# Optimization experiments

Measured on AMD Instinct MI355X. Metric: run time of the kernel, lower is better.

The kernel has to match this reference:

```python
import jax, jax.numpy as jnp
import numpy as np
from jax import lax

B, T, L, HID = 128, 8, 8, 64  # batch, horizon(=num_layers), lstm layers, hidden

def setup_inputs() -> dict:
    key = jax.random.key(0)
    ks = jax.random.split(key, 40)
    def rn(i, shape, s=0.02):
        return jax.random.normal(ks[i], shape, dtype=jnp.float32) * s
    inp = {
        'image_data': jax.random.normal(ks[0], (B, 3, 192, 256), jnp.float32),
        'action_input_data': jax.random.normal(ks[1], (B, T, 2), jnp.float32),
        'ground_truth_data': jax.random.normal(ks[2], (B, T, 6), jnp.float32),
        'conv1_w': rn(3, (32, 3, 5, 5)), 'conv1_b': rn(4, (32,)),
        'conv2_w': rn(5, (64, 32, 3, 3)), 'conv2_b': rn(6, (64,)),
        'conv3_w': rn(7, (64, 64, 3, 3)), 'conv3_b': rn(8, (64,)),
        'fc1_w': rn(9, (256, 42240)), 'fc1_b': rn(10, (256,)),
        'fc2_w': rn(11, (128, 256)), 'fc2_b': rn(12, (128,)),
        'lowd1_w': rn(13, (128, 128)), 'lowd1_b': rn(14, (128,)),
        'lowd2_w': rn(15, (128, 128)), 'lowd2_b': rn(16, (128,)),
        'act1_w': rn(17, (16, 2)), 'act1_b': rn(18, (16,)),
        'act2_w': rn(19, (16, 16)), 'act2_b': rn(20, (16,)),
        'lstm_Wih0': rn(21, (4 * HID, 16)),
        'lstm_Wih': rn(22, (L - 1, 4 * HID, HID)),
        'lstm_Whh': rn(23, (L, 4 * HID, HID)),
        'lstm_bih': rn(24, (L, 4 * HID)),
        'lstm_bhh': rn(25, (L, 4 * HID)),
        'out1_w': rn(26, (32, 64)), 'out1_b': rn(27, (32,)),
        'out2_w': rn(28, (4, 32)), 'out2_b': rn(29, (4,)),
        'BATCH_SIZE': B, 'horizon': T,
    }
    return inp

def _lin(x, w, b):
    return x @ w.T + b

def _conv(x, w, b):
    y = lax.conv_general_dilated(x, w, (2, 2), 'VALID',
                                 dimension_numbers=('NCHW', 'OIHW', 'NCHW'))
    return y + b[None, :, None, None]

def _lstm(x, h0, c0, Wih0, Wih, Whh, bih, bhh):
    # x: (B,T,16); h0/c0: (L,B,HID). PyTorch gate order: i,f,g,o.
    inp = x
    for l in range(L):
        Wih_l = Wih0 if l == 0 else Wih[l - 1]
        bih_l, bhh_l, Whh_l = bih[l], bhh[l], Whh[l]
        def step(carry, xt):
            h, c = carry
            g = xt @ Wih_l.T + bih_l + h @ Whh_l.T + bhh_l
            i_, f_, g_, o_ = jnp.split(g, 4, axis=-1)
            c = jax.nn.sigmoid(f_) * c + jax.nn.sigmoid(i_) * jnp.tanh(g_)
            h = jax.nn.sigmoid(o_) * jnp.tanh(c)
            return (h, c), h
        _, ys = lax.scan(step, (h0[l], c0[l]), jnp.swapaxes(inp, 0, 1))
        inp = jnp.swapaxes(ys, 0, 1)  # (B,T,HID)
    return inp

def reference(image_data, action_input_data, ground_truth_data,
              conv1_w, conv1_b, conv2_w, conv2_b, conv3_w, conv3_b,
              fc1_w, fc1_b, fc2_w, fc2_b,
              lowd1_w, lowd1_b, lowd2_w, lowd2_b,
              act1_w, act1_b, act2_w, act2_b,
              lstm_Wih0, lstm_Wih, lstm_Whh, lstm_bih, lstm_bhh,
              out1_w, out1_b, out2_w, out2_b,
              BATCH_SIZE, horizon):
    # CNN image pipeline
    x = jax.nn.relu(_conv(image_data, conv1_w, conv1_b))
    x = jax.nn.relu(_conv(x, conv2_w, conv2_b))
    x = _conv(x, conv3_w, conv3_b)
    x = x.reshape(x.shape[0], -1)  # (B, 42240)
    x = jax.nn.relu(_lin(x, fc1_w, fc1_b))
    cnn_out1 = _lin(x, fc2_w, fc2_b)  # (B,128)
    cnn_out2 = _lin(jax.nn.relu(_lin(cnn_out1, lowd1_w, lowd1_b)), lowd2_w, lowd2_b)
    # action pipeline
    a = _lin(jax.nn.relu(_lin(action_input_data, act1_w, act1_b)), act2_w, act2_b)
    # split: first 64 -> c0, second 64 -> h0; broadcast over layers
    c_tmp, h_tmp = cnn_out2[:, :HID], cnn_out2[:, HID:]
    h0 = jnp.broadcast_to(h_tmp[None], (L, h_tmp.shape[0], HID))
    c0 = jnp.broadcast_to(c_tmp[None], (L, c_tmp.shape[0], HID))
    lstm_out = _lstm(a, h0, c0, lstm_Wih0, lstm_Wih, lstm_Whh, lstm_bih, lstm_bhh)
    mo = _lin(jax.nn.relu(_lin(lstm_out, out1_w, out1_b)), out2_w, out2_b)  # (B,T,4)
    # batched yaw rotation (vectorizes the original per-sample loop)
    yaw = ground_truth_data[:, 0, 5]
    cy, sy = jnp.cos(yaw), jnp.sin(yaw)
    z, o = jnp.zeros_like(cy), jnp.ones_like(cy)
    rot = jnp.stack([cy, -sy, z, sy, cy, z, z, z, o], axis=-1).reshape(-1, 3, 3)
    pos = jnp.einsum('bti,bij->btj', mo[:, :, :3], rot) + ground_truth_data[:, 0, 1:4][:, None, :]
    return jnp.concatenate([pos, mo[:, :, 3:4]], axis=-1)
```

## Files before the change

### kernel.cpp

```cpp
#include <hip/hip_runtime.h>
#include <cstdint>

#define DEV __device__ __forceinline__

typedef __attribute__((ext_vector_type(8))) short bf16x8;
typedef __attribute__((ext_vector_type(4))) float f32x4;
typedef __attribute__((ext_vector_type(2))) __fp16 h2t;
typedef __attribute__((ext_vector_type(4))) unsigned int u32x4;
typedef unsigned long long u64;

DEV unsigned short f2bf(float f) {
    unsigned u = __float_as_uint(f);
    unsigned r = u + 0x7fffu + ((u >> 16) & 1u);
    return (unsigned short)(r >> 16);
}
DEV uint32_t pkbf2(float a, float b) {
    return (uint32_t)f2bf(a) | ((uint32_t)f2bf(b) << 16);
}
DEV uint32_t pkh2(float a, float b) {
    h2t p = __builtin_amdgcn_cvt_pkrtz(a, b);
    union { h2t h; uint32_t u; } c;
    c.h = p;
    return c.u;
}
DEV float dot2(uint32_t w, uint32_t x, float acc) {
    union { uint32_t u; h2t h; } a, b;
    a.u = w; b.u = x;
    return __builtin_amdgcn_fdot2(a.h, b.h, acc, false);
}
DEV float sigm(float x) { return __builtin_amdgcn_rcpf(1.f + __expf(-x)); }
DEV float tanh_(float x) { return fmaf(2.f, sigm(2.f * x), -1.f); }
DEV uint32_t packpair(float h) {
    float hs = __int_as_float(__builtin_amdgcn_ds_swizzle(__float_as_int(h), 0x041F));
    return pkh2(h, hs);
}
DEV uint32_t comp4v(u32x4 v, int e) {
    return (e == 0) ? v[0] : (e == 1) ? v[1] : (e == 2) ? v[2] : v[3];
}
DEV u64 pack4bf(float a, float b, float c, float d) {
    unsigned lo = (unsigned)f2bf(a) | ((unsigned)f2bf(b) << 16);
    unsigned hi = (unsigned)f2bf(c) | ((unsigned)f2bf(d) << 16);
    return (u64)lo | ((u64)hi << 32);
}

__global__ __launch_bounds__(256) void k_wprep(const float* __restrict__ w1,
                                               const float* __restrict__ w2,
                                               const float* __restrict__ w3,
                                               unsigned short* __restrict__ w1t,
                                               unsigned short* __restrict__ w2t,
                                               unsigned short* __restrict__ w3t) {
    int i = blockIdx.x * 256 + threadIdx.x;
    if (i < 32 * 128) {
        int oc = i >> 7, k = i & 127;
        int cc = k >> 3, u = (k >> 2) & 1, c = k & 3;
        int r = cc / 3, kx = 2 * (cc - 3 * r) + u;
        w1t[i] = (cc < 15 && kx < 5 && c < 3) ? f2bf(w1[oc * 75 + c * 25 + r * 5 + kx])
                                              : (unsigned short)0;
    } else if (i < 32 * 128 + 64 * 288) {
        int j = i - 32 * 128;
        int oc = j / 288, k = j - oc * 288;
        int pos = k >> 5, c = k & 31;
        int ocr = ((c >> 2) & 1) * 16 + (c >> 3) * 4 + (c & 3);
        w2t[j] = f2bf(w2[oc * 288 + ocr * 9 + pos]);
    } else if (i < 32 * 128 + 64 * 288 + 64 * 576) {
        int j = i - 32 * 128 - 64 * 288;
        int oc = j / 576, k = j - oc * 576;
        int pos = k >> 6, c = k & 63;
        w3t[j] = f2bf(w3[oc * 576 + c * 9 + pos]);
    }
}

__global__ __launch_bounds__(256) void k_wprep_lstm(const float* __restrict__ Wih0,
                                                    const float* __restrict__ Wih,
                                                    const float* __restrict__ Whh,
                                                    uint32_t* __restrict__ wpk) {
    int idx = blockIdx.x * 256 + threadIdx.x;
    int lane = idx & 63;
    int j = (idx >> 6) & 63;
    int l = idx >> 12;
    int g = j >> 4, q = j & 15;
    int r = g * 64 + lane;
    uint32_t ov[4];
#pragma unroll
    for (int e = 0; e < 4; ++e) {
        int p = q * 4 + e;
        float w0, w1;
        if (p < 32) {
            int k0 = 2 * p;
            if (l == 0) {
                w0 = (k0 < 16) ? Wih0[r * 16 + k0] : 0.f;
                w1 = (k0 + 1 < 16) ? Wih0[r * 16 + k0 + 1] : 0.f;
            } else {
                const float* base = Wih + ((size_t)(l - 1) * 256 + r) * 64;
                w0 = base[k0];
                w1 = base[k0 + 1];
            }
        } else {
            int k0 = 2 * (p - 32);
            const float* base = Whh + ((size_t)l * 256 + r) * 64;
            w0 = base[k0];
            w1 = base[k0 + 1];
        }
        ov[e] = pkh2(w0, w1);
    }
    uint4 v;
    v.x = ov[0]; v.y = ov[1]; v.z = ov[2]; v.w = ov[3];
    ((uint4*)wpk)[idx] = v;
}

__global__ __launch_bounds__(256, 1) void k_conv12(const float* __restrict__ img,
                                                   const unsigned short* __restrict__ w1t,
                                                   const float* __restrict__ b1,
                                                   const unsigned short* __restrict__ w2t,
                                                   const float* __restrict__ b2,
                                                   unsigned short* __restrict__ out) {
    int b = blockIdx.x, xh = blockIdx.y, yh = blockIdx.z;
    int tid = threadIdx.x;
    int w = tid >> 6, lane = tid & 63;
    int quad = lane >> 4, nl = lane & 15;
    int nh = w >> 1, rw = w & 1;
    __shared__ __align__(16) char ldsI[8 * 2080];
    __shared__ __align__(16) char ldsC[4 * 4536];
    const float* ib = img + (size_t)b * 3 * 192 * 256;
    int y0 = yh * 23;
    int imx = 124 * xh + tid;
    bool stg = tid < 132;

    bf16x8 wa1[4], wb1[4];
#pragma unroll
    for (int ks = 0; ks < 4; ++ks) {
        wa1[ks] = *(const bf16x8*)(w1t + nl * 128 + ks * 32 + quad * 8);
        wb1[ks] = *(const bf16x8*)(w1t + (16 + nl) * 128 + ks * 32 + quad * 8);
    }
    bf16x8 wa2[9], wb2[9];
#pragma unroll
    for (int ks = 0; ks < 9; ++ks) {
        wa2[ks] = *(const bf16x8*)(w2t + ((rw * 2 + 0) * 16 + nl) * 288 + ks * 32 + quad * 8);
        wb2[ks] = *(const bf16x8*)(w2t + ((rw * 2 + 1) * 16 + nl) * 288 + ks * 32 + quad * 8);
    }
    float4 c1b0 = *(const float4*)(b1 + quad * 4);
    float4 c1b1 = *(const float4*)(b1 + 16 + quad * 4);
    float4 c2b0 = *(const float4*)(b2 + (rw * 2 + 0) * 16 + quad * 4);
    float4 c2b1 = *(const float4*)(b2 + (rw * 2 + 1) * 16 + quad * 4);

    auto ldimg = [&](int row, float& f0, float& f1, float& f2) {
        if (row > 191) row = 191;
        const float* ip = ib + row * 256 + imx;
        f0 = ip[0];
        f1 = ip[192 * 256];
        f2 = ip[2 * 192 * 256];
    };
    auto stimg = [&](int row, float f0, float f1, float f2) {
        uint32_t lo = (uint32_t)f2bf(f0) | ((uint32_t)f2bf(f1) << 16);
        *(u64*)(ldsI + (row & 7) * 2080 + imx * 8) = (u64)lo | ((u64)f2bf(f2) << 32);
    };
    auto conv1row = [&](int R1) {
        f32x4 a00, a01;
        a00[0] = c1b0.x; a00[1] = c1b0.y; a00[2] = c1b0.z; a00[3] = c1b0.w;
        a01[0] = c1b1.x; a01[1] = c1b1.y; a01[2] = c1b1.z; a01[3] = c1b1.w;
        f32x4 a10 = a00, a11 = a01;
#pragma unroll
        for (int ks = 0; ks < 4; ++ks) {
            int cc = ks * 4 + quad;
            int r = cc / 3, kxp = cc - 3 * r;
            int rb = ((2 * R1 + r) & 7) * 2080 + 992 * xh + 512 * nh + kxp * 16 + nl * 16;
            bf16x8 v0 = *(const bf16x8*)(ldsI + rb);
            bf16x8 v1 = *(const bf16x8*)(ldsI + rb + 256);
            a00 = __builtin_amdgcn_mfma_f32_16x16x32_bf16(wa1[ks], v0, a00, 0, 0, 0);
            a01 = __builtin_amdgcn_mfma_f32_16x16x32_bf16(wb1[ks], v0, a01, 0, 0, 0);
            a10 = __builtin_amdgcn_mfma_f32_16x16x32_bf16(wa1[ks], v1, a10, 0, 0, 0);
            a11 = __builtin_amdgcn_mfma_f32_16x16x32_bf16(wb1[ks], v1, a11, 0, 0, 0);
        }
        int cs = (R1 & 3) * 4536;
        int xl0 = nh * 32 + nl;
        {
            u64 lo = pack4bf(fmaxf(a00[0], 0.f), fmaxf(a00[1], 0.f),
                             fmaxf(a00[2], 0.f), fmaxf(a00[3], 0.f));
            u64 hi = pack4bf(fmaxf(a01[0], 0.f), fmaxf(a01[1], 0.f),
                             fmaxf(a01[2], 0.f), fmaxf(a01[3], 0.f));
            uint4 st;
            st.x = (uint32_t)lo; st.y = (uint32_t)(lo >> 32);
            st.z = (uint32_t)hi; st.w = (uint32_t)(hi >> 32);
            *(uint4*)(ldsC + cs + xl0 * 72 + quad * 16) = st;
        }
        int xl1 = xl0 + 16;
        if (xl1 < 63) {
            u64 lo = pack4bf(fmaxf(a10[0], 0.f), fmaxf(a10[1], 0.f),
                             fmaxf(a10[2], 0.f), fmaxf(a10[3], 0.f));
            u64 hi = pack4bf(fmaxf(a11[0], 0.f), fmaxf(a11[1], 0.f),
                             fmaxf(a11[2], 0.f), fmaxf(a11[3], 0.f));
            uint4 st;
            st.x = (uint32_t)lo; st.y = (uint32_t)(lo >> 32);
            st.z = (uint32_t)hi; st.w = (uint32_t)(hi >> 32);
            *(uint4*)(ldsC + cs + xl1 * 72 + quad * 16) = st;
        }
    };

    {
        float p0[8], p1[8], p2[8];
        if (stg) {
#pragma unroll
            for (int r = 0; r < 8; ++r) ldimg(4 * y0 + r, p0[r], p1[r], p2[r]);
        }
        __builtin_amdgcn_sched_barrier(0);
        if (stg) {
#pragma unroll
            for (int r = 0; r < 8; ++r) stimg(4 * y0 + r, p0[r], p1[r], p2[r]);
        }
    }
    __syncthreads();
    conv1row(2 * y0 + rw);
    float g0[4], g1[4], g2[4];
    if (stg) {
#pragma unroll
        for (int r = 0; r < 4; ++r) ldimg(4 * y0 + 8 + r, g0[r], g1[r], g2[r]);
    }
    __syncthreads();
    if (stg) {
#pragma unroll
        for (int r = 0; r < 4; ++r) stimg(4 * y0 + 8 + r, g0[r], g1[r], g2[r]);
    }
    __syncthreads();

    for (int t = 0; t < 23; ++t) {
        int y = y0 + t;
        conv1row(2 * y + 2 + rw);
        if (stg) {
#pragma unroll
            for (int r = 0; r < 4; ++r) ldimg(4 * y + 12 + r, g0[r], g1[r], g2[r]);
        }
        __syncthreads();
        {
            f32x4 acc0, acc1;
            acc0[0] = c2b0.x; acc0[1] = c2b0.y; acc0[2] = c2b0.z; acc0[3] = c2b0.w;
            acc1[0] = c2b1.x; acc1[1] = c2b1.y; acc1[2] = c2b1.z; acc1[3] = c2b1.w;
            int xl = nh * 16 + nl;
#pragma unroll
            for (int ks = 0; ks < 9; ++ks) {
                int r = ks / 3, kx = ks - r * 3;
                const char* base = ldsC + ((2 * y + r) & 3) * 4536 + (2 * xl + kx) * 72 + quad * 16;
                union { u64 d[2]; bf16x8 v; } bb;
                bb.d[0] = *(const u64*)(base);
                bb.d[1] = *(const u64*)(base + 8);
                acc0 = __builtin_amdgcn_mfma_f32_16x16x32_bf16(wa2[ks], bb.v, acc0, 0, 0, 0);
                acc1 = __builtin_amdgcn_mfma_f32_16x16x32_bf16(wb2[ks], bb.v, acc1, 0, 0, 0);
            }
            if (xl < 31) {
                int xg = xh * 31 + xl;
                u64 q0 = pack4bf(fmaxf(acc0[0], 0.f), fmaxf(acc0[1], 0.f),
                                 fmaxf(acc0[2], 0.f), fmaxf(acc0[3], 0.f));
                u64 q1 = pack4bf(fmaxf(acc1[0], 0.f), fmaxf(acc1[1], 0.f),
                                 fmaxf(acc1[2], 0.f), fmaxf(acc1[3], 0.f));
                *(u64*)(out + (((size_t)b * 46 + y) * 62 + xg) * 64 + (rw * 2 + 0) * 16 + quad * 4) = q0;
                *(u64*)(out + (((size_t)b * 46 + y) * 62 + xg) * 64 + (rw * 2 + 1) * 16 + quad * 4) = q1;
            }
        }
        if (stg) {
#pragma unroll
            for (int r = 0; r < 4; ++r) stimg(4 * y + 12 + r, g0[r], g1[r], g2[r]);
        }
        __syncthreads();
    }
}

__global__ __launch_bounds__(256, 1) void k_conv3m(const unsigned short* __restrict__ in,
                                                   const unsigned short* __restrict__ w3t,
                                                   const float* __restrict__ bias,
                                                   unsigned short* __restrict__ out) {
    int b = blockIdx.x, xh = blockIdx.y, yh = blockIdx.z;
    int tid = threadIdx.x;
    int wave = tid >> 6, lane = tid & 63;
    int quad = lane >> 4, nl = lane & 15;
    __shared__ __align__(16) char lds[4 * 4488];
    const u64* in64 = (const u64*)in;

    bf16x8 wf[18];
#pragma unroll
    for (int ks = 0; ks < 18; ++ks)
        wf[ks] = *(const bf16x8*)(w3t + (wave * 16 + nl) * 576 + ks * 32 + quad * 8);
    float4 bv = *(const float4*)(bias + wave * 16 + quad * 4);

    int y0 = yh * 11;
    int rr = tid >> 7, li = tid & 127;

    {
        int y2 = 2 * y0 + rr;
        const u64* s = in64 + ((size_t)(b * 46 + y2) * 62 + 30 * xh) * 16;
        int slot = y2 & 3;
        u64 g0[4];
#pragma unroll
        for (int j = 0; j < 4; ++j) { int idx = li + j * 128; g0[j] = (idx < 496) ? s[idx] : 0ull; }
#pragma unroll
        for (int j = 0; j < 4; ++j) {
            int idx = li + j * 128;
            if (idx < 496) *(u64*)(lds + slot * 4488 + (idx >> 4) * 136 + (idx & 15) * 8) = g0[j];
        }
        int y2b = 2 * y0 + 2;
        const u64* s2 = in64 + ((size_t)(b * 46 + y2b) * 62 + 30 * xh) * 16;
        int slot2 = y2b & 3;
        u64 g1[2];
#pragma unroll
        for (int j = 0; j < 2; ++j) { int idx = tid + j * 256; g1[j] = (idx < 496) ? s2[idx] : 0ull; }
#pragma unroll
        for (int j = 0; j < 2; ++j) {
            int idx = tid + j * 256;
            if (idx < 496) *(u64*)(lds + slot2 * 4488 + (idx >> 4) * 136 + (idx & 15) * 8) = g1[j];
        }
    }
    u64 g[4];
    {
        int y2 = 2 * y0 + 3 + rr;
        const u64* s = in64 + ((size_t)(b * 46 + y2) * 62 + 30 * xh) * 16;
#pragma unroll
        for (int j = 0; j < 4; ++j) { int idx = li + j * 128; g[j] = (idx < 496) ? s[idx] : 0ull; }
    }
    __syncthreads();

    for (int yy = 0; yy < 11; ++yy) {
        int y = y0 + yy;
        f32x4 acc;
        acc[0] = bv.x; acc[1] = bv.y; acc[2] = bv.z; acc[3] = bv.w;
        int sb0 = ((2 * y) & 3) * 4488;
        int sb1 = ((2 * y + 1) & 3) * 4488;
        int sb2 = ((2 * y + 2) & 3) * 4488;
#pragma unroll
        for (int ks = 0; ks < 18; ++ks) {
            const int pos = ks >> 1, half = ks & 1;
            const int r = pos / 3, kx = pos - r * 3;
            int sb = (r == 0) ? sb0 : (r == 1) ? sb1 : sb2;
            union { u64 d[2]; bf16x8 v; } bb;
            const char* base = lds + sb + (2 * nl + kx) * 136 + half * 64 + quad * 16;
            bb.d[0] = *(const u64*)(base);
            bb.d[1] = *(const u64*)(base + 8);
            acc = __builtin_amdgcn_mfma_f32_16x16x32_bf16(wf[ks], bb.v, acc, 0, 0, 0);
        }
        if (nl < 15) {
            int xg = xh * 15 + nl;
#pragma unroll
            for (int r2 = 0; r2 < 4; ++r2)
                out[(size_t)b * 42240 + (wave * 16 + quad * 4 + r2) * 660 + y * 30 + xg] = f2bf(acc[r2]);
        }
        __syncthreads();
        {
            int row = 2 * y + 3 + rr;
            int slot = row & 3;
#pragma unroll
            for (int j = 0; j < 4; ++j) {
                int idx = li + j * 128;
                if (idx < 496) *(u64*)(lds + slot * 4488 + (idx >> 4) * 136 + (idx & 15) * 8) = g[j];
            }
        }
        if (yy < 10) {
            int y2 = 2 * y + 5 + rr;
            if (y2 > 45) y2 = 45;
            const u64* s = in64 + ((size_t)(b * 46 + y2) * 62 + 30 * xh) * 16;
#pragma unroll
            for (int j = 0; j < 4; ++j) { int idx = li + j * 128; g[j] = (idx < 496) ? s[idx] : 0ull; }
        }
        __syncthreads();
    }
}

__global__ __launch_bounds__(256) void k_fc1_mfma(const unsigned short* __restrict__ A,
                                                  const float* __restrict__ W,
                                                  float* __restrict__ part) {
    int kc = blockIdx.x;
    int nb = blockIdx.y;
    int tid = threadIdx.x;
    int wave = tid >> 6, lane = tid & 63;
    int m16 = lane & 15, quad = lane >> 4;
    __shared__ __align__(16) char lw[2][64 * 80];
    __shared__ __align__(16) char la[2][128 * 80];
    int k0 = kc * 704;
    int wrow = tid >> 2, wseg = tid & 3;
    const float* wsrc = W + (size_t)(nb * 64 + wrow) * 42240 + k0 + wseg * 8;
    int arow = tid >> 1, aseg = tid & 1;
    const uint4* asrc = (const uint4*)(A + (size_t)arow * 42240 + k0) + aseg * 2;
    float4 wr0 = ((const float4*)wsrc)[0];
    float4 wr1 = ((const float4*)wsrc)[1];
    uint4 ar0 = asrc[0];
    uint4 ar1 = asrc[1];
    f32x4 acc[8] = {};
    for (int ks = 0; ks < 22; ++ks) {
        int buf = ks & 1;
        uint4 wp;
        wp.x = pkbf2(wr0.x, wr0.y); wp.y = pkbf2(wr0.z, wr0.w);
        wp.z = pkbf2(wr1.x, wr1.y); wp.w = pkbf2(wr1.z, wr1.w);
        *(uint4*)(lw[buf] + wrow * 80 + wseg * 16) = wp;
        *(uint4*)(la[buf] + arow * 80 + aseg * 32) = ar0;
        *(uint4*)(la[buf] + arow * 80 + aseg * 32 + 16) = ar1;
        if (ks < 21) {
            wsrc += 32;
            asrc += 4;
            wr0 = ((const float4*)wsrc)[0];
            wr1 = ((const float4*)wsrc)[1];
            ar0 = asrc[0];
            ar1 = asrc[1];
        }
        __syncthreads();
        bf16x8 wf = *(const bf16x8*)(lw[buf] + (wave * 16 + m16) * 80 + quad * 16);
        const char* lab = la[buf] + m16 * 80 + quad * 16;
#pragma unroll
        for (int tm = 0; tm < 8; ++tm) {
            bf16x8 af = *(const bf16x8*)(lab + tm * 16 * 80);
            acc[tm] = __builtin_amdgcn_mfma_f32_16x16x32_bf16(af, wf, acc[tm], 0, 0, 0);
        }
    }
    int n = nb * 64 + wave * 16 + m16;
    float* pb = part + ((size_t)kc * 128) * 256 + n;
#pragma unroll
    for (int tm = 0; tm < 8; ++tm) {
        int row = tm * 16 + quad * 4;
#pragma unroll
        for (int r = 0; r < 4; ++r) pb[(size_t)(row + r) * 256] = acc[tm][r];
    }
}

__global__ __launch_bounds__(256) void k_head(const float* __restrict__ part,
                                              const float* __restrict__ f1b,
                                              const float* __restrict__ w2, const float* __restrict__ b2,
                                              const float* __restrict__ lw1, const float* __restrict__ lb1,
                                              const float* __restrict__ lw2, const float* __restrict__ lb2,
                                              float* __restrict__ cnn2) {
    int b = blockIdx.x, t = threadIdx.x;
    __shared__ float xa[256];
    __shared__ float xb[128];
    __shared__ float xc[128];
    __shared__ float pp[256];
    float s = f1b[t];
#pragma unroll
    for (int kc = 0; kc < 60; ++kc) s += part[((size_t)kc * 128 + b) * 256 + t];
    xa[t] = fmaxf(s, 0.f);
    __syncthreads();
    int n = t & 127, half = t >> 7;
    float acc = half ? 0.f : b2[n];
    {
        const float* w2r = w2 + n * 256 + half * 128;
        const float* xar = xa + half * 128;
#pragma unroll
        for (int k = 0; k < 128; ++k) acc = fmaf(xar[k], w2r[k], acc);
    }
    pp[t] = acc;
    __syncthreads();
    if (t < 128) xb[t] = pp[t] + pp[t + 128];
    __syncthreads();
    acc = half ? 0.f : lb1[n];
    {
        const float* l1r = lw1 + n * 128 + half * 64;
        const float* xbr = xb + half * 64;
#pragma unroll
        for (int k = 0; k < 64; ++k) acc = fmaf(xbr[k], l1r[k], acc);
    }
    pp[t] = acc;
    __syncthreads();
    if (t < 128) xc[t] = fmaxf(pp[t] + pp[t + 128], 0.f);
    __syncthreads();
    acc = half ? 0.f : lb2[n];
    {
        const float* l2r = lw2 + n * 128 + half * 64;
        const float* xcr = xc + half * 64;
#pragma unroll
        for (int k = 0; k < 64; ++k) acc = fmaf(xcr[k], l2r[k], acc);
    }
    pp[t] = acc;
    __syncthreads();
    if (t < 128) cnn2[b * 128 + t] = pp[t] + pp[t + 128];
}

__global__ __launch_bounds__(256) void k_act(const float* __restrict__ ain,
                                             const float* __restrict__ w1, const float* __restrict__ b1,
                                             const float* __restrict__ w2, const float* __restrict__ b2,
                                             float* __restrict__ abuf) {
    int idx = blockIdx.x * 256 + threadIdx.x;
    float x0 = ain[idx * 2], x1 = ain[idx * 2 + 1];
    float h1[16];
#pragma unroll
    for (int i = 0; i < 16; ++i)
        h1[i] = fmaxf(fmaf(x0, w1[i * 2], fmaf(x1, w1[i * 2 + 1], b1[i])), 0.f);
#pragma unroll
    for (int i = 0; i < 16; ++i) {
        float a = b2[i];
#pragma unroll
        for (int j = 0; j < 16; ++j) a = fmaf(h1[j], w2[i * 16 + j], a);
        abuf[idx * 16 + i] = a;
    }
}

__global__ __launch_bounds__(512, 2) void k_lstm(const float* __restrict__ abuf,
                                                 const float* __restrict__ cnn2,
                                                 const uint32_t* __restrict__ wpk,
                                                 const float* __restrict__ bih,
                                                 const float* __restrict__ bhh,
                                                 float* __restrict__ lout) {
    int b = blockIdx.x;
    int tid = threadIdx.x;
    int w = tid >> 6, lane = tid & 63;
    int sl = w >> 1, pt = w & 1;
    __shared__ uint32_t hbuf[2][3][32];
    __shared__ uint32_t h3pk[8][32];
    __shared__ float4 pex[8][64];

    uint32_t xq[8];
#pragma unroll
    for (int t = 0; t < 8; ++t) {
        float x0 = 0.f, x1 = 0.f;
        if (lane < 8) {
            const float* ap = abuf + (b * 8 + t) * 16 + 2 * lane;
            x0 = ap[0];
            x1 = ap[1];
        }
        xq[t] = pkh2(x0, x1);
    }
    float h0 = cnn2[b * 128 + 64 + lane];
    float c0 = cnn2[b * 128 + lane];
    const u32x4* wbase = (const u32x4*)wpk;

#pragma unroll
    for (int P = 0; P < 2; ++P) {
        const int L = P * 4 + sl;
        u32x4 wreg[4][8];
#pragma unroll
        for (int g = 0; g < 4; ++g)
#pragma unroll
            for (int q = 0; q < 8; ++q)
                wreg[g][q] = wbase[(size_t)L * 4096 + (g * 16 + pt * 8 + q) * 64 + lane];
        float bias0 = 0.f, bias1 = 0.f, bias2 = 0.f, bias3 = 0.f;
        if (pt == 0) {
            bias0 = bih[L * 256 + lane] + bhh[L * 256 + lane];
            bias1 = bih[L * 256 + 64 + lane] + bhh[L * 256 + 64 + lane];
            bias2 = bih[L * 256 + 128 + lane] + bhh[L * 256 + 128 + lane];
            bias3 = bih[L * 256 + 192 + lane] + bhh[L * 256 + 192 + lane];
        }
        float h = h0, c = c0;
        uint32_t hpk = packpair(h0);

        for (int s = 0; s < 11; ++s) {
            bool act = (s >= sl && s < sl + 8);
            float a0 = bias0, a1 = bias1, a2 = bias2, a3 = bias3;
            if (act) {
                if (pt == 0) {
                    uint32_t xcur;
                    if (sl == 0)
                        xcur = (P == 0) ? xq[0] : h3pk[s][lane & 31];
                    else
                        xcur = hbuf[(s & 1) ^ 1][sl - 1][lane & 31];
#pragma unroll
                    for (int m = 0; m < 32; ++m) {
                        uint32_t bx = (uint32_t)__builtin_amdgcn_readlane((int)xcur, m);
                        int q = m >> 2, e = m & 3;
                        a0 = dot2(comp4v(wreg[0][q], e), bx, a0);
                        a1 = dot2(comp4v(wreg[1][q], e), bx, a1);
                        a2 = dot2(comp4v(wreg[2][q], e), bx, a2);
                        a3 = dot2(comp4v(wreg[3][q], e), bx, a3);
                    }
                } else {
#pragma unroll
                    for (int m = 0; m < 32; ++m) {
                        uint32_t bh2 = (uint32_t)__builtin_amdgcn_readlane((int)hpk, 2 * m);
                        int q = m >> 2, e = m & 3;
                        a0 = dot2(comp4v(wreg[0][q], e), bh2, a0);
                        a1 = dot2(comp4v(wreg[1][q], e), bh2, a1);
                        a2 = dot2(comp4v(wreg[2][q], e), bh2, a2);
                        a3 = dot2(comp4v(wreg[3][q], e), bh2, a3);
                    }
                }
                float4 pv;
                pv.x = a0; pv.y = a1; pv.z = a2; pv.w = a3;
                pex[w][lane] = pv;
            }
            __syncthreads();
            if (act) {
                float4 po = pex[w ^ 1][lane];
                float g0 = a0 + po.x, g1 = a1 + po.y, g2 = a2 + po.z, g3 = a3 + po.w;
                float gi = sigm(g0), gf = sigm(g1), gv = tanh_(g2), go = sigm(g3);
                c = gf * c + gi * gv;
                h = go * tanh_(c);
                hpk = packpair(h);
                if (pt == 0) {
                    if (sl < 3) {
                        if (!(lane & 1)) hbuf[s & 1][sl][lane >> 1] = hpk;
                    } else if (P == 0) {
                        if (!(lane & 1)) h3pk[s - 3][lane >> 1] = hpk;
                    } else {
                        lout[((size_t)b * 8 + (s - 3)) * 64 + lane] = h;
                    }
                }
            }
            if (P == 0 && w == 0) {
#pragma unroll
                for (int k = 0; k < 7; ++k) xq[k] = xq[k + 1];
            }
            __syncthreads();
        }
    }
}

__global__ __launch_bounds__(256) void k_out(const float* __restrict__ lout,
                                             const float* __restrict__ w1, const float* __restrict__ b1,
                                             const float* __restrict__ w2, const float* __restrict__ b2,
                                             const float* __restrict__ gt, float* __restrict__ out) {
    int idx = blockIdx.x * 256 + threadIdx.x;
    int b = idx >> 3;
    float x[64];
#pragma unroll
    for (int j = 0; j < 64; ++j) x[j] = lout[idx * 64 + j];
    float h[32];
#pragma unroll 8
    for (int i = 0; i < 32; ++i) {
        float a = b1[i];
#pragma unroll
        for (int j = 0; j < 64; ++j) a = fmaf(x[j], w1[i * 64 + j], a);
        h[i] = fmaxf(a, 0.f);
    }
    float mo[4];
#pragma unroll
    for (int i = 0; i < 4; ++i) {
        float a = b2[i];
#pragma unroll
        for (int j = 0; j < 32; ++j) a = fmaf(h[j], w2[i * 32 + j], a);
        mo[i] = a;
    }
    float yaw = gt[b * 48 + 5];
    float cy = cosf(yaw), sy = sinf(yaw);
    out[idx * 4 + 0] = fmaf(mo[0], cy, fmaf(mo[1], sy, gt[b * 48 + 1]));
    out[idx * 4 + 1] = fmaf(mo[0], -sy, fmaf(mo[1], cy, gt[b * 48 + 2]));
    out[idx * 4 + 2] = mo[2] + gt[b * 48 + 3];
    out[idx * 4 + 3] = mo[3];
}

extern "C" void kernel_launch(void* const* d_in, const int* in_sizes, int n_in,
                              void* d_out, int out_size, void* d_ws, size_t ws_size,
                              hipStream_t stream) {
    const float* img = (const float*)d_in[0];
    const float* ain = (const float*)d_in[1];
    const float* gt = (const float*)d_in[2];
    const float* c1w = (const float*)d_in[3];
    const float* c1b = (const float*)d_in[4];
    const float* c2w = (const float*)d_in[5];
    const float* c2b = (const float*)d_in[6];
    const float* c3w = (const float*)d_in[7];
    const float* c3b = (const float*)d_in[8];
    const float* f1w = (const float*)d_in[9];
    const float* f1b = (const float*)d_in[10];
    const float* f2w = (const float*)d_in[11];
    const float* f2b = (const float*)d_in[12];
    const float* l1w = (const float*)d_in[13];
    const float* l1b = (const float*)d_in[14];
    const float* l2w = (const float*)d_in[15];
    const float* l2b = (const float*)d_in[16];
    const float* a1w = (const float*)d_in[17];
    const float* a1b = (const float*)d_in[18];
    const float* a2w = (const float*)d_in[19];
    const float* a2b = (const float*)d_in[20];
    const float* wih0 = (const float*)d_in[21];
    const float* wih = (const float*)d_in[22];
    const float* whh = (const float*)d_in[23];
    const float* bihp = (const float*)d_in[24];
    const float* bhhp = (const float*)d_in[25];
    const float* o1w = (const float*)d_in[26];
    const float* o1b = (const float*)d_in[27];
    const float* o2w = (const float*)d_in[28];
    const float* o2b = (const float*)d_in[29];
    float* out = (float*)d_out;

    char* ws = (char*)d_ws;
    unsigned short* c2o = (unsigned short*)(ws + 97026048);
    unsigned short* c3o = (unsigned short*)(ws + 143753216);
    float* f1p = (float*)(ws + 154566656);
    float* cnn2 = (float*)(ws + 163348480);
    float* abuf = (float*)(ws + 163414016);
    float* lo = (float*)(ws + 163479552);
    unsigned short* w1t = (unsigned short*)(ws + 163741696);
    unsigned short* w2t = (unsigned short*)(ws + 163749888);
    unsigned short* w3t = (unsigned short*)(ws + 163786752);
    uint32_t* wpk = (uint32_t*)(ws + 163860480);

    k_wprep<<<232, 256, 0, stream>>>(c1w, c2w, c3w, w1t, w2t, w3t);
    k_wprep_lstm<<<128, 256, 0, stream>>>(wih0, wih, whh, wpk);
    k_conv12<<<dim3(128, 2, 2), 256, 0, stream>>>(img, w1t, c1b, w2t, c2b, c2o);
    k_conv3m<<<dim3(128, 2, 2), 256, 0, stream>>>(c2o, w3t, c3b, c3o);
    k_fc1_mfma<<<dim3(60, 4), 256, 0, stream>>>(c3o, f1w, f1p);
    k_head<<<128, 256, 0, stream>>>(f1p, f1b, f2w, f2b, l1w, l1b, l2w, l2b, cnn2);
    k_act<<<4, 256, 0, stream>>>(ain, a1w, a1b, a2w, a2b, abuf);
    k_lstm<<<128, 512, 0, stream>>>(abuf, cnn2, wpk, bihp, bhhp, lo);
    k_out<<<4, 256, 0, stream>>>(lo, o1w, o1b, o2w, o2b, gt, out);
}
```

Before: 331.8 us.

## Split conv1+conv2 into four row slices with deeper ring buffers and one barrier per step

The fused conv1/conv2 kernel now splits output rows into four slices instead of two, doubling the grid to 1024 blocks, and allows two blocks per CU. The image and conv1 staging buffers become 12- and 6-slot rings. One conv1 row is computed ahead so each loop step needs only one barrier instead of two. The aim is more parallelism and fewer synchronisations per row, at the cost of more LDS per block, more recomputed halo rows at slice edges, and more complex slot indexing.

```diff
diff --git a/kernel.cpp b/kernel.cpp
--- a/kernel.cpp
+++ b/kernel.cpp
@@ -108,21 +108,22 @@
     ((uint4*)wpk)[idx] = v;
 }
 
-__global__ __launch_bounds__(256, 1) void k_conv12(const float* __restrict__ img,
+__global__ __launch_bounds__(256, 2) void k_conv12(const float* __restrict__ img,
                                                    const unsigned short* __restrict__ w1t,
                                                    const float* __restrict__ b1,
                                                    const unsigned short* __restrict__ w2t,
                                                    const float* __restrict__ b2,
                                                    unsigned short* __restrict__ out) {
-    int b = blockIdx.x, xh = blockIdx.y, yh = blockIdx.z;
+    int b = blockIdx.x, xh = blockIdx.y, ys = blockIdx.z;
     int tid = threadIdx.x;
     int w = tid >> 6, lane = tid & 63;
     int quad = lane >> 4, nl = lane & 15;
     int nh = w >> 1, rw = w & 1;
-    __shared__ __align__(16) char ldsI[8 * 2080];
-    __shared__ __align__(16) char ldsC[4 * 4536];
+    __shared__ __align__(16) char ldsI[12 * 2080];
+    __shared__ __align__(16) char ldsC[6 * 4536];
     const float* ib = img + (size_t)b * 3 * 192 * 256;
-    int y0 = yh * 23;
+    int y0 = ys * 12;
+    int NT = (ys == 3) ? 10 : 12;
     int imx = 124 * xh + tid;
     bool stg = tid < 132;
 
@@ -150,11 +151,11 @@
         f1 = ip[192 * 256];
         f2 = ip[2 * 192 * 256];
     };
-    auto stimg = [&](int row, float f0, float f1, float f2) {
+    auto stimgS = [&](int slot, float f0, float f1, float f2) {
         uint32_t lo = (uint32_t)f2bf(f0) | ((uint32_t)f2bf(f1) << 16);
-        *(u64*)(ldsI + (row & 7) * 2080 + imx * 8) = (u64)lo | ((u64)f2bf(f2) << 32);
+        *(u64*)(ldsI + slot * 2080 + imx * 8) = (u64)lo | ((u64)f2bf(f2) << 32);
     };
-    auto conv1row = [&](int R1) {
+    auto conv1row = [&](int s0, int cslot) {
         f32x4 a00, a01;
         a00[0] = c1b0.x; a00[1] = c1b0.y; a00[2] = c1b0.z; a00[3] = c1b0.w;
         a01[0] = c1b1.x; a01[1] = c1b1.y; a01[2] = c1b1.z; a01[3] = c1b1.w;
@@ -163,7 +164,8 @@
         for (int ks = 0; ks < 4; ++ks) {
             int cc = ks * 4 + quad;
             int r = cc / 3, kxp = cc - 3 * r;
-            int rb = ((2 * R1 + r) & 7) * 2080 + 992 * xh + 512 * nh + kxp * 16 + nl * 16;
+            int sl = s0 + r; if (sl >= 12) sl -= 12;
+            int rb = sl * 2080 + 992 * xh + 512 * nh + kxp * 16 + nl * 16;
             bf16x8 v0 = *(const bf16x8*)(ldsI + rb);
             bf16x8 v1 = *(const bf16x8*)(ldsI + rb + 256);
             a00 = __builtin_amdgcn_mfma_f32_16x16x32_bf16(wa1[ks], v0, a00, 0, 0, 0);
@@ -171,7 +173,7 @@
             a10 = __builtin_amdgcn_mfma_f32_16x16x32_bf16(wa1[ks], v1, a10, 0, 0, 0);
             a11 = __builtin_amdgcn_mfma_f32_16x16x32_bf16(wb1[ks], v1, a11, 0, 0, 0);
         }
-        int cs = (R1 & 3) * 4536;
+        int cs = cslot * 4536;
         int xl0 = nh * 32 + nl;
         {
             u64 lo = pack4bf(fmaxf(a00[0], 0.f), fmaxf(a00[1], 0.f),
@@ -197,39 +199,46 @@
     };
 
     {
-        float p0[8], p1[8], p2[8];
+        float p0[12], p1[12], p2[12];
         if (stg) {
 #pragma unroll
-            for (int r = 0; r < 8; ++r) ldimg(4 * y0 + r, p0[r], p1[r], p2[r]);
+            for (int r = 0; r < 12; ++r) ldimg(4 * y0 + r, p0[r], p1[r], p2[r]);
         }
         __builtin_amdgcn_sched_barrier(0);
         if (stg) {
 #pragma unroll
-            for (int r = 0; r < 8; ++r) stimg(4 * y0 + r, p0[r], p1[r], p2[r]);
-        }
-    }
-    __syncthreads();
-    conv1row(2 * y0 + rw);
+            for (int r = 0; r < 12; ++r) stimgS(r, p0[r], p1[r], p2[r]);
+        }
+    }
+    __syncthreads();
+    conv1row(2 * rw, rw);
     float g0[4], g1[4], g2[4];
     if (stg) {
 #pragma unroll
-        for (int r = 0; r < 4; ++r) ldimg(4 * y0 + 8 + r, g0[r], g1[r], g2[r]);
-    }
-    __syncthreads();
+        for (int j = 0; j < 4; ++j) ldimg(4 * y0 + 12 + j, g0[j], g1[j], g2[j]);
+    }
+    __syncthreads();
+    conv1row(4 + 2 * rw, 2 + rw);
     if (stg) {
 #pragma unroll
-        for (int r = 0; r < 4; ++r) stimg(4 * y0 + 8 + r, g0[r], g1[r], g2[r]);
-    }
-    __syncthreads();
-
-    for (int t = 0; t < 23; ++t) {
+        for (int j = 0; j < 4; ++j) stimgS(j, g0[j], g1[j], g2[j]);
+    }
+    __syncthreads();
+
+    int t3 = 0;
+    for (int t = 0; t < NT; ++t) {
         int y = y0 + t;
-        conv1row(2 * y + 2 + rw);
+        int t3h = t3 >> 1;
         if (stg) {
 #pragma unroll
-            for (int r = 0; r < 4; ++r) ldimg(4 * y + 12 + r, g0[r], g1[r], g2[r]);
-        }
-        __syncthreads();
+            for (int j = 0; j < 4; ++j) ldimg(4 * y + 16 + j, g0[j], g1[j], g2[j]);
+        }
+        int R1 = 2 * y + 4 + rw;
+        if (R1 <= 93) {
+            int s0 = t3 + 8 + 2 * rw; if (s0 >= 12) s0 -= 12;
+            int cs = t3h + 4 + rw; if (cs >= 6) cs -= 6;
+            conv1row(s0, cs);
+        }
         {
             f32x4 acc0, acc1;
             acc0[0] = c2b0.x; acc0[1] = c2b0.y; acc0[2] = c2b0.z; acc0[3] = c2b0.w;
@@ -238,7 +247,8 @@
 #pragma unroll
             for (int ks = 0; ks < 9; ++ks) {
                 int r = ks / 3, kx = ks - r * 3;
-                const char* base = ldsC + ((2 * y + r) & 3) * 4536 + (2 * xl + kx) * 72 + quad * 16;
+                int cs = t3h + r; if (cs >= 6) cs -= 6;
+                const char* base = ldsC + cs * 4536 + (2 * xl + kx) * 72 + quad * 16;
                 union { u64 d[2]; bf16x8 v; } bb;
                 bb.d[0] = *(const u64*)(base);
                 bb.d[1] = *(const u64*)(base + 8);
@@ -257,9 +267,13 @@
         }
         if (stg) {
 #pragma unroll
-            for (int r = 0; r < 4; ++r) stimg(4 * y + 12 + r, g0[r], g1[r], g2[r]);
+            for (int j = 0; j < 4; ++j) {
+                int sl = t3 + 4 + j; if (sl >= 12) sl -= 12;
+                stimgS(sl, g0[j], g1[j], g2[j]);
+            }
         }
         __syncthreads();
+        t3 += 4; if (t3 == 12) t3 = 0;
     }
 }
 
@@ -677,7 +691,7 @@
 
     k_wprep<<<232, 256, 0, stream>>>(c1w, c2w, c3w, w1t, w2t, w3t);
     k_wprep_lstm<<<128, 256, 0, stream>>>(wih0, wih, whh, wpk);
-    k_conv12<<<dim3(128, 2, 2), 256, 0, stream>>>(img, w1t, c1b, w2t, c2b, c2o);
+    k_conv12<<<dim3(128, 2, 4), 256, 0, stream>>>(img, w1t, c1b, w2t, c2b, c2o);
     k_conv3m<<<dim3(128, 2, 2), 256, 0, stream>>>(c2o, w3t, c3b, c3o);
     k_fc1_mfma<<<dim3(60, 4), 256, 0, stream>>>(c3o, f1w, f1p);
     k_head<<<128, 256, 0, stream>>>(f1p, f1b, f2w, f2b, l1w, l1b, l2w, l2b, cnn2);
```

Result: no change. 327.0 us (-1.4%).

## Deepen conv1/conv2 LDS ring buffers and prefetch image rows two stages ahead

Applied to the files above, without the earlier changes.

The fused conv1+conv2 kernel now uses 16-row image and 8-row conv1 LDS rings. Image rows are loaded two iterations ahead with ping-pong registers, which removes one of the two __syncthreads per output row. The software bf16 rounding is replaced by the hardware v_cvt_pk_bf16_f32 instruction, and launch bounds ask for 2 blocks per CU. LDS per block roughly doubles (about 69KB), which may limit co-residency, and the 2-block hint may add register pressure or spilling.

```diff
diff --git a/kernel.cpp b/kernel.cpp
--- a/kernel.cpp
+++ b/kernel.cpp
@@ -16,6 +16,11 @@
 }
 DEV uint32_t pkbf2(float a, float b) {
     return (uint32_t)f2bf(a) | ((uint32_t)f2bf(b) << 16);
+}
+DEV uint32_t cvtpk(float lo, float hi) {
+    uint32_t r;
+    asm("v_cvt_pk_bf16_f32 %0, %1, %2" : "=v"(r) : "v"(lo), "v"(hi));
+    return r;
 }
 DEV uint32_t pkh2(float a, float b) {
     h2t p = __builtin_amdgcn_cvt_pkrtz(a, b);
@@ -108,21 +113,21 @@
     ((uint4*)wpk)[idx] = v;
 }
 
-__global__ __launch_bounds__(256, 1) void k_conv12(const float* __restrict__ img,
+__global__ __launch_bounds__(256, 2) void k_conv12(const float* __restrict__ img,
                                                    const unsigned short* __restrict__ w1t,
                                                    const float* __restrict__ b1,
                                                    const unsigned short* __restrict__ w2t,
                                                    const float* __restrict__ b2,
                                                    unsigned short* __restrict__ out) {
-    int b = blockIdx.x, xh = blockIdx.y, yh = blockIdx.z;
+    int b = blockIdx.x, xh = blockIdx.y, ys = blockIdx.z;
     int tid = threadIdx.x;
     int w = tid >> 6, lane = tid & 63;
     int quad = lane >> 4, nl = lane & 15;
     int nh = w >> 1, rw = w & 1;
-    __shared__ __align__(16) char ldsI[8 * 2080];
-    __shared__ __align__(16) char ldsC[4 * 4536];
+    __shared__ __align__(16) char ldsI[16 * 2080];
+    __shared__ __align__(16) char ldsC[8 * 4536];
     const float* ib = img + (size_t)b * 3 * 192 * 256;
-    int y0 = yh * 23;
+    int y0 = ys * 23;
     int imx = 124 * xh + tid;
     bool stg = tid < 132;
 
@@ -150,20 +155,21 @@
         f1 = ip[192 * 256];
         f2 = ip[2 * 192 * 256];
     };
-    auto stimg = [&](int row, float f0, float f1, float f2) {
-        uint32_t lo = (uint32_t)f2bf(f0) | ((uint32_t)f2bf(f1) << 16);
-        *(u64*)(ldsI + (row & 7) * 2080 + imx * 8) = (u64)lo | ((u64)f2bf(f2) << 32);
+    auto stimgS = [&](int row, float f0, float f1, float f2) {
+        uint32_t lo = cvtpk(f0, f1);
+        *(u64*)(ldsI + (row & 15) * 2080 + imx * 8) = (u64)lo | ((u64)cvtpk(f2, 0.f) << 32);
     };
     auto conv1row = [&](int R1) {
         f32x4 a00, a01;
         a00[0] = c1b0.x; a00[1] = c1b0.y; a00[2] = c1b0.z; a00[3] = c1b0.w;
         a01[0] = c1b1.x; a01[1] = c1b1.y; a01[2] = c1b1.z; a01[3] = c1b1.w;
         f32x4 a10 = a00, a11 = a01;
+        int base2 = 2 * R1;
 #pragma unroll
         for (int ks = 0; ks < 4; ++ks) {
             int cc = ks * 4 + quad;
             int r = cc / 3, kxp = cc - 3 * r;
-            int rb = ((2 * R1 + r) & 7) * 2080 + 992 * xh + 512 * nh + kxp * 16 + nl * 16;
+            int rb = ((base2 + r) & 15) * 2080 + 992 * xh + 512 * nh + kxp * 16 + nl * 16;
             bf16x8 v0 = *(const bf16x8*)(ldsI + rb);
             bf16x8 v1 = *(const bf16x8*)(ldsI + rb + 256);
             a00 = __builtin_amdgcn_mfma_f32_16x16x32_bf16(wa1[ks], v0, a00, 0, 0, 0);
@@ -171,30 +177,28 @@
             a10 = __builtin_amdgcn_mfma_f32_16x16x32_bf16(wa1[ks], v1, a10, 0, 0, 0);
             a11 = __builtin_amdgcn_mfma_f32_16x16x32_bf16(wb1[ks], v1, a11, 0, 0, 0);
         }
-        int cs = (R1 & 3) * 4536;
+        int cs = (R1 & 7) * 4536;
         int xl0 = nh * 32 + nl;
         {
-            u64 lo = pack4bf(fmaxf(a00[0], 0.f), fmaxf(a00[1], 0.f),
-                             fmaxf(a00[2], 0.f), fmaxf(a00[3], 0.f));
-            u64 hi = pack4bf(fmaxf(a01[0], 0.f), fmaxf(a01[1], 0.f),
-                             fmaxf(a01[2], 0.f), fmaxf(a01[3], 0.f));
             uint4 st;
-            st.x = (uint32_t)lo; st.y = (uint32_t)(lo >> 32);
-            st.z = (uint32_t)hi; st.w = (uint32_t)(hi >> 32);
+            st.x = cvtpk(fmaxf(a00[0], 0.f), fmaxf(a00[1], 0.f));
+            st.y = cvtpk(fmaxf(a00[2], 0.f), fmaxf(a00[3], 0.f));
+            st.z = cvtpk(fmaxf(a01[0], 0.f), fmaxf(a01[1], 0.f));
+            st.w = cvtpk(fmaxf(a01[2], 0.f), fmaxf(a01[3], 0.f));
             *(uint4*)(ldsC + cs + xl0 * 72 + quad * 16) = st;
         }
         int xl1 = xl0 + 16;
         if (xl1 < 63) {
-            u64 lo = pack4bf(fmaxf(a10[0], 0.f), fmaxf(a10[1], 0.f),
-                             fmaxf(a10[2], 0.f), fmaxf(a10[3], 0.f));
-            u64 hi = pack4bf(fmaxf(a11[0], 0.f), fmaxf(a11[1], 0.f),
-                             fmaxf(a11[2], 0.f), fmaxf(a11[3], 0.f));
             uint4 st;
-            st.x = (uint32_t)lo; st.y = (uint32_t)(lo >> 32);
-            st.z = (uint32_t)hi; st.w = (uint32_t)(hi >> 32);
+            st.x = cvtpk(fmaxf(a10[0], 0.f), fmaxf(a10[1], 0.f));
+            st.y = cvtpk(fmaxf(a10[2], 0.f), fmaxf(a10[3], 0.f));
+            st.z = cvtpk(fmaxf(a11[0], 0.f), fmaxf(a11[1], 0.f));
+            st.w = cvtpk(fmaxf(a11[2], 0.f), fmaxf(a11[3], 0.f));
             *(uint4*)(ldsC + cs + xl1 * 72 + quad * 16) = st;
         }
     };
+
+    float A0[4], A1[4], A2[4], B0[4], B1[4], B2[4];
 
     {
         float p0[8], p1[8], p2[8];
@@ -205,31 +209,33 @@
         __builtin_amdgcn_sched_barrier(0);
         if (stg) {
 #pragma unroll
-            for (int r = 0; r < 8; ++r) stimg(4 * y0 + r, p0[r], p1[r], p2[r]);
+            for (int r = 0; r < 8; ++r) stimgS(4 * y0 + r, p0[r], p1[r], p2[r]);
+#pragma unroll
+            for (int r = 0; r < 8; ++r) ldimg(4 * y0 + 8 + r, p0[r], p1[r], p2[r]);
+        }
+        __builtin_amdgcn_sched_barrier(0);
+        if (stg) {
+#pragma unroll
+            for (int r = 0; r < 8; ++r) stimgS(4 * y0 + 8 + r, p0[r], p1[r], p2[r]);
+#pragma unroll
+            for (int j = 0; j < 4; ++j) ldimg(4 * y0 + 16 + j, A0[j], A1[j], A2[j]);
         }
     }
     __syncthreads();
     conv1row(2 * y0 + rw);
-    float g0[4], g1[4], g2[4];
-    if (stg) {
-#pragma unroll
-        for (int r = 0; r < 4; ++r) ldimg(4 * y0 + 8 + r, g0[r], g1[r], g2[r]);
-    }
-    __syncthreads();
-    if (stg) {
-#pragma unroll
-        for (int r = 0; r < 4; ++r) stimg(4 * y0 + 8 + r, g0[r], g1[r], g2[r]);
-    }
-    __syncthreads();
-
-    for (int t = 0; t < 23; ++t) {
-        int y = y0 + t;
-        conv1row(2 * y + 2 + rw);
+    conv1row(2 * y0 + 2 + rw);
+    __syncthreads();
+
+    auto iter = [&](int y, float (&W0)[4], float (&W1)[4], float (&W2)[4],
+                    float (&L0)[4], float (&L1)[4], float (&L2)[4]) {
         if (stg) {
 #pragma unroll
-            for (int r = 0; r < 4; ++r) ldimg(4 * y + 12 + r, g0[r], g1[r], g2[r]);
-        }
-        __syncthreads();
+            for (int j = 0; j < 4; ++j) stimgS(4 * y + 16 + j, W0[j], W1[j], W2[j]);
+#pragma unroll
+            for (int j = 0; j < 4; ++j) ldimg(4 * y + 20 + j, L0[j], L1[j], L2[j]);
+        }
+        int R1 = 2 * y + 4 + rw;
+        if (R1 <= 93) conv1row(R1);
         {
             f32x4 acc0, acc1;
             acc0[0] = c2b0.x; acc0[1] = c2b0.y; acc0[2] = c2b0.z; acc0[3] = c2b0.w;
@@ -238,7 +244,7 @@
 #pragma unroll
             for (int ks = 0; ks < 9; ++ks) {
                 int r = ks / 3, kx = ks - r * 3;
-                const char* base = ldsC + ((2 * y + r) & 3) * 4536 + (2 * xl + kx) * 72 + quad * 16;
+                const char* base = ldsC + ((2 * y + r) & 7) * 4536 + (2 * xl + kx) * 72 + quad * 16;
                 union { u64 d[2]; bf16x8 v; } bb;
                 bb.d[0] = *(const u64*)(base);
                 bb.d[1] = *(const u64*)(base + 8);
@@ -247,20 +253,22 @@
             }
             if (xl < 31) {
                 int xg = xh * 31 + xl;
-                u64 q0 = pack4bf(fmaxf(acc0[0], 0.f), fmaxf(acc0[1], 0.f),
-                                 fmaxf(acc0[2], 0.f), fmaxf(acc0[3], 0.f));
-                u64 q1 = pack4bf(fmaxf(acc1[0], 0.f), fmaxf(acc1[1], 0.f),
-                                 fmaxf(acc1[2], 0.f), fmaxf(acc1[3], 0.f));
+                u64 q0 = (u64)cvtpk(fmaxf(acc0[0], 0.f), fmaxf(acc0[1], 0.f)) |
+                         ((u64)cvtpk(fmaxf(acc0[2], 0.f), fmaxf(acc0[3], 0.f)) << 32);
+                u64 q1 = (u64)cvtpk(fmaxf(acc1[0], 0.f), fmaxf(acc1[1], 0.f)) |
+                         ((u64)cvtpk(fmaxf(acc1[2], 0.f), fmaxf(acc1[3], 0.f)) << 32);
                 *(u64*)(out + (((size_t)b * 46 + y) * 62 + xg) * 64 + (rw * 2 + 0) * 16 + quad * 4) = q0;
                 *(u64*)(out + (((size_t)b * 46 + y) * 62 + xg) * 64 + (rw * 2 + 1) * 16 + quad * 4) = q1;
             }
         }
-        if (stg) {
-#pragma unroll
-            for (int r = 0; r < 4; ++r) stimg(4 * y + 12 + r, g0[r], g1[r], g2[r]);
-        }
         __syncthreads();
-    }
+    };
+
+    for (int t = 0; t + 1 < 23; t += 2) {
+        iter(y0 + t, A0, A1, A2, B0, B1, B2);
+        iter(y0 + t + 1, B0, B1, B2, A0, A1, A2);
+    }
+    iter(y0 + 22, A0, A1, A2, B0, B1, B2);
 }
 
 __global__ __launch_bounds__(256, 1) void k_conv3m(const unsigned short* __restrict__ in,
```

Result: faster. 319.0 us (-3.8%).
